# Kernel optimization log

Hardware: AMD Instinct MI355X
Metric: run time of the kernel (lower is better)

The kernel has to match this reference:

```python
import jax, jax.numpy as jnp
import numpy as np

B, S, D, H = 4, 2048, 1024, 16
HD = D // H


def setup_inputs() -> dict:
    key = jax.random.key(0)
    k1, k2, k3 = jax.random.split(key, 3)
    x = jax.random.normal(k1, (B, S, D), dtype=jnp.float32)
    w_qkv = jax.random.normal(k2, (D, 3 * D), dtype=jnp.float32) * (1.0 / np.sqrt(D))
    w_out = jax.random.normal(k3, (D, D), dtype=jnp.float32) * (1.0 / np.sqrt(D))
    return {"x": x, "w_qkv": w_qkv, "w_out": w_out}


def reference(x, w_qkv, w_out):
    bsz, seq_len, d = x.shape
    qkv = x @ w_qkv  # [B, S, 3D]
    q, k, v = jnp.split(qkv, 3, axis=-1)
    # [B, H, S, HD]
    q = q.reshape(bsz, seq_len, H, HD).transpose(0, 2, 1, 3)
    k = k.reshape(bsz, seq_len, H, HD).transpose(0, 2, 1, 3)
    v = v.reshape(bsz, seq_len, H, HD).transpose(0, 2, 1, 3)
    scale = 1.0 / np.sqrt(HD)
    scores = jnp.einsum('bhqd,bhkd->bhqk', q, k) * scale  # [B, H, S, S]
    causal = jnp.tril(jnp.ones((seq_len, seq_len), dtype=bool))
    scores = jnp.where(causal[None, None], scores, -jnp.inf)
    weights = jax.nn.softmax(scores, axis=-1)
    ctx = jnp.einsum('bhqk,bhkd->bhqd', weights, v)
    ctx = ctx.transpose(0, 2, 1, 3).reshape(bsz, seq_len, d)
    return ctx @ w_out
```

## Files before the change

### kernel.cpp

```cpp
#include <hip/hip_runtime.h>
#include <stdint.h>

typedef unsigned short u16;
typedef __attribute__((ext_vector_type(4))) float f32x4;
typedef __attribute__((ext_vector_type(8))) __bf16 bf16x8;
typedef __attribute__((ext_vector_type(8))) u16 u16x8;
typedef __attribute__((ext_vector_type(4))) u16 u16x4;
typedef __attribute__((ext_vector_type(2))) unsigned u32x2;

static constexpr int kB = 4, kS = 2048, kD = 1024, kH = 16, kHD = 64;
static constexpr int M1 = kB * kS;
static constexpr int N1 = 3 * kD;
static constexpr int K1 = kD;

#define SCLF 0.18033688011112042f
#define MFMA16(a, b, c) __builtin_amdgcn_mfma_f32_16x16x32_bf16((a), (b), (c), 0, 0, 0)

union U4 { unsigned u[4]; bf16x8 v; };

__device__ __forceinline__ u16 f2bf(float f) {
  union { float f; uint32_t u; } c; c.f = f;
  uint32_t u = c.u + 0x7FFFu + ((c.u >> 16) & 1u);
  return (u16)(u >> 16);
}

__device__ __forceinline__ unsigned pkbf(float a, float b) {
  union { __bf16 h[2]; unsigned u; } c;
  c.h[0] = (__bf16)a; c.h[1] = (__bf16)b;
  return c.u;
}

__device__ __forceinline__ void gload_lds16(const u16* g, u16* l) {
  __builtin_amdgcn_global_load_lds(
      (const __attribute__((address_space(1))) unsigned int*)g,
      (__attribute__((address_space(3))) unsigned int*)l, 16, 0, 0);
}

__global__ __launch_bounds__(256) void k_cast_x(const float* __restrict__ x,
                                                u16* __restrict__ o) {
  int i = (blockIdx.x * 256 + threadIdx.x) * 4;
  f32x4 v = *(const f32x4*)(x + i);
  u16x4 r;
  r[0] = f2bf(v[0]); r[1] = f2bf(v[1]); r[2] = f2bf(v[2]); r[3] = f2bf(v[3]);
  *(u16x4*)(o + i) = r;
}

__global__ __launch_bounds__(256) void k_transpose_cast(const float* __restrict__ w,
                                                        u16* __restrict__ wt,
                                                        int K, int N) {
  __shared__ float t[32][33];
  const int n0 = blockIdx.x * 32, k0 = blockIdx.y * 32;
  const int tx = threadIdx.x & 31, ty = threadIdx.x >> 5;
  for (int r = ty; r < 32; r += 8)
    t[r][tx] = w[(size_t)(k0 + r) * N + n0 + tx];
  __syncthreads();
  for (int r = ty; r < 32; r += 8)
    wt[(size_t)(n0 + r) * K + k0 + tx] = f2bf(t[tx][r]);
}

template <int MODE>
__global__ __launch_bounds__(512) void k_gemm_bt(const u16* __restrict__ A,
                                                 const u16* __restrict__ BT,
                                                 u16* __restrict__ obf,
                                                 float* __restrict__ of,
                                                 int M, int N, int K) {
  __shared__ __align__(16) u16 Asb[3][128 * 64];
  __shared__ __align__(16) u16 Bsb[3][256 * 64];

  const int tid = threadIdx.x;
  const int wave = tid >> 6, lane = tid & 63;
  const int l15 = lane & 15, l16 = lane >> 4;

  const int bid = blockIdx.x;
  const int qch = gridDim.x >> 3;
  const int swz = (bid & 7) * qch + (bid >> 3);
  const int ntN = N >> 8;
  const int row0 = (swz / ntN) * 128, col0 = (swz % ntN) * 256;
  const int wm = (wave >> 2) * 64, wn = (wave & 3) * 64;

  f32x4 acc[4][4];
#pragma unroll
  for (int i = 0; i < 4; ++i)
#pragma unroll
    for (int j = 0; j < 4; ++j) acc[i][j] = f32x4{0.f, 0.f, 0.f, 0.f};

  const int lr = lane >> 3, ls = lane & 7;
  const u16* srcA[2];
#pragma unroll
  for (int j = 0; j < 2; ++j) {
    const int r = (wave * 2 + j) * 8 + lr;
    srcA[j] = A + (size_t)(row0 + r) * K + (ls ^ (r & 7)) * 8;
  }
  const u16* srcB[4];
#pragma unroll
  for (int j = 0; j < 4; ++j) {
    const int r = (wave * 4 + j) * 8 + lr;
    srcB[j] = BT + (size_t)(col0 + r) * K + (ls ^ (r & 7)) * 8;
  }

  const int nT = K >> 6;

#define STAGE(t)                                                        \
  {                                                                     \
    const int buf_ = (t) % 3;                                           \
    const int kt_ = (t) * 64;                                           \
    _Pragma("unroll")                                                   \
    for (int j = 0; j < 2; ++j)                                         \
      gload_lds16(srcA[j] + kt_, &Asb[buf_][(wave * 2 + j) * 512]);     \
    _Pragma("unroll")                                                   \
    for (int j = 0; j < 4; ++j)                                         \
      gload_lds16(srcB[j] + kt_, &Bsb[buf_][(wave * 4 + j) * 512]);     \
  }

  STAGE(0);
  STAGE(1);

  for (int t = 0; t < nT; ++t) {
    if (t + 1 < nT) asm volatile("s_waitcnt vmcnt(6)" ::: "memory");
    else            asm volatile("s_waitcnt vmcnt(0)" ::: "memory");
    __builtin_amdgcn_s_barrier();
    __builtin_amdgcn_sched_barrier(0);

    if (t + 2 < nT) STAGE(t + 2);

    const u16* As = &Asb[t % 3][0];
    const u16* Bs = &Bsb[t % 3][0];
#pragma unroll
    for (int kk = 0; kk < 2; ++kk) {
      bf16x8 af[4], bfv[4];
#pragma unroll
      for (int f = 0; f < 4; ++f) {
        const int ra = wm + f * 16 + l15;
        af[f] = *(const bf16x8*)&As[ra * 64 + (((kk * 4 + l16) ^ (ra & 7)) * 8)];
        const int rb = wn + f * 16 + l15;
        bfv[f] = *(const bf16x8*)&Bs[rb * 64 + (((kk * 4 + l16) ^ (rb & 7)) * 8)];
      }
      __builtin_amdgcn_s_setprio(1);
#pragma unroll
      for (int fm = 0; fm < 4; ++fm)
#pragma unroll
        for (int fn = 0; fn < 4; ++fn)
          acc[fm][fn] = MFMA16(af[fm], bfv[fn], acc[fm][fn]);
      __builtin_amdgcn_s_setprio(0);
    }
  }

#pragma unroll
  for (int fm = 0; fm < 4; ++fm)
#pragma unroll
    for (int fn = 0; fn < 4; ++fn) {
      const int n = col0 + wn + fn * 16 + l15;
#pragma unroll
      for (int j = 0; j < 4; ++j) {
        const int m = row0 + wm + fm * 16 + l16 * 4 + j;
        float v = acc[fm][fn][j];
        if constexpr (MODE == 0) {
          const int which = n >> 10, d = n & 1023;
          const int h = d >> 6, hd = d & 63;
          const int b = m >> 11, s = m & 2047;
          if (which == 0) v *= SCLF;
          obf[((((size_t)which * 4 + b) * 16 + h) * 2048 + s) * 64 + hd] = f2bf(v);
        } else {
          of[(size_t)m * N + n] = v;
        }
      }
    }
#undef STAGE
}

__global__ __launch_bounds__(512, 4) void k_attn(const u16* __restrict__ Qg,
                                                 const u16* __restrict__ Kg,
                                                 const u16* __restrict__ Vg,
                                                 u16* __restrict__ ctx) {
  __shared__ __align__(16) u16 Ks[2][64 * 64];
  __shared__ __align__(16) unsigned Vt[2][2048];
  __shared__ __align__(16) unsigned Pl[8 * 256];

  const int bid = blockIdx.x;
  const int xcd = bid & 7, i2 = bid >> 3;
  const int bh = xcd * 8 + (i2 & 7);
  const int p = i2 >> 3;
  const int bb = bh >> 4, hh = bh & 15;
  const int tid = threadIdx.x;
  const int wave = tid >> 6, lane = tid & 63;
  const int l15 = lane & 15, l16 = lane >> 4;

  const u16* Qb = Qg + (size_t)bh * kS * kHD;
  const u16* Kb = Kg + (size_t)bh * kS * kHD;
  const u16* Vb = Vg + (size_t)bh * kS * kHD;

  const int kkey = tid >> 3, ksl = tid & 7;
  const int do4 = tid & 15, kp = tid >> 4;
  unsigned* Pw = Pl + wave * 256 + l15 * 16;
  const int pm = ((l15 >> 1) & 3) << 2;

  unsigned voff[4];
#pragma unroll
  for (int i = 0; i < 4; ++i) {
    const int d = do4 * 4 + i;
    voff[i] = d * 32 + (kp ^ ((((d & 7) ^ (d >> 3))) << 2));
  }
  const u16* ksrc = Kb + (size_t)kkey * 64 + (ksl ^ (kkey & 7)) * 8;

  for (int phase = 0; phase < 2; ++phase) {
    const int qsup = phase ? (15 - p) : p;
    const int qstart = qsup * 128 + wave * 16;
    const int ntiles = 2 * qsup + 2;

    bf16x8 bq[2];
#pragma unroll
    for (int ds = 0; ds < 2; ++ds)
      bq[ds] = *(const bf16x8*)(Qb + (size_t)(qstart + l15) * 64 + ds * 32 + l16 * 8);

    f32x4 acc[4];
#pragma unroll
    for (int i = 0; i < 4; ++i) acc[i] = f32x4{0.f, 0.f, 0.f, 0.f};
    float mrow = -3e38f, lrowh = 0.f;

    __syncthreads();

    u16x4 va, vb;
    {
      const u16* vs = Vb + (size_t)(2 * kp) * 64 + do4 * 4;
      va = *(const u16x4*)vs; vb = *(const u16x4*)(vs + 64);
    }
#pragma unroll
    for (int i = 0; i < 4; ++i)
      Vt[0][voff[i]] = (unsigned)va[i] | ((unsigned)vb[i] << 16);
    {
      const u16* vs = Vb + (size_t)(64 + 2 * kp) * 64 + do4 * 4;
      va = *(const u16x4*)vs; vb = *(const u16x4*)(vs + 64);
    }
    gload_lds16(ksrc, &Ks[0][wave * 512]);

    for (int t = 0; t < ntiles; ++t) {
      const int kv0 = t * 64;
      __syncthreads();

      if (t + 1 < ntiles) {
        const int nb = (t + 1) & 1;
#pragma unroll
        for (int i = 0; i < 4; ++i)
          Vt[nb][voff[i]] = (unsigned)va[i] | ((unsigned)vb[i] << 16);
        gload_lds16(ksrc + (size_t)(t + 1) * 64 * 64, &Ks[nb][wave * 512]);
        if (t + 2 < ntiles) {
          const u16* vs = Vb + (size_t)((t + 2) * 64 + 2 * kp) * 64 + do4 * 4;
          va = *(const u16x4*)vs; vb = *(const u16x4*)(vs + 64);
        }
      }

      if (kv0 > qstart + 15) continue;

      const u16* Ksb = &Ks[t & 1][0];
      const unsigned* Vtb = &Vt[t & 1][0];
      const int qv = qstart + l15;
      const bool have1 = (kv0 + 32 <= qstart + 15);

      f32x4 stA0 = f32x4{0.f, 0.f, 0.f, 0.f}, stA1 = stA0;
      f32x4 stB0 = stA0, stB1 = stA0;
      __builtin_amdgcn_s_setprio(1);
#pragma unroll
      for (int ds = 0; ds < 2; ++ds) {
        const int slot = ((ds * 4 + l16) ^ (l15 & 7)) * 8;
        bf16x8 ak0 = *(const bf16x8*)&Ksb[(l15) * 64 + slot];
        stA0 = MFMA16(ak0, bq[ds], stA0);
        bf16x8 ak1 = *(const bf16x8*)&Ksb[(16 + l15) * 64 + slot];
        stA1 = MFMA16(ak1, bq[ds], stA1);
        if (have1) {
          bf16x8 bk0 = *(const bf16x8*)&Ksb[(32 + l15) * 64 + slot];
          stB0 = MFMA16(bk0, bq[ds], stB0);
          bf16x8 bk1 = *(const bf16x8*)&Ksb[(48 + l15) * 64 + slot];
          stB1 = MFMA16(bk1, bq[ds], stB1);
        }
      }
      __builtin_amdgcn_s_setprio(0);

      if (kv0 + 31 > qstart) {
#pragma unroll
        for (int j = 0; j < 4; ++j) {
          const int key = kv0 + l16 * 4 + j;
          stA0[j] = (key <= qv) ? stA0[j] : -3e38f;
          stA1[j] = (key + 16 <= qv) ? stA1[j] : -3e38f;
        }
      }
      if (have1 && (kv0 + 63 > qstart)) {
#pragma unroll
        for (int j = 0; j < 4; ++j) {
          const int key = kv0 + 32 + l16 * 4 + j;
          stB0[j] = (key <= qv) ? stB0[j] : -3e38f;
          stB1[j] = (key + 16 <= qv) ? stB1[j] : -3e38f;
        }
      }

      float tl = fmaxf(fmaxf(fmaxf(stA0[0], stA0[1]), fmaxf(stA0[2], stA0[3])),
                       fmaxf(fmaxf(stA1[0], stA1[1]), fmaxf(stA1[2], stA1[3])));
      if (have1) {
        tl = fmaxf(tl, fmaxf(fmaxf(stB0[0], stB0[1]), fmaxf(stB0[2], stB0[3])));
        tl = fmaxf(tl, fmaxf(fmaxf(stB1[0], stB1[1]), fmaxf(stB1[2], stB1[3])));
      }

      float mn;
      if (__all(tl <= mrow + 8.0f)) {
        mn = mrow;
      } else {
        float tj = fmaxf(tl, __shfl_xor(tl, 16, 64));
        tj = fmaxf(tj, __shfl_xor(tj, 32, 64));
        mn = fmaxf(mrow, tj);
        const float al = exp2f(mrow - mn);
        mrow = mn;
        lrowh *= al;
#pragma unroll
        for (int i = 0; i < 4; ++i)
#pragma unroll
          for (int j = 0; j < 4; ++j) acc[i][j] *= al;
      }

      {
#pragma unroll
        for (int j = 0; j < 4; ++j) {
          stA0[j] = exp2f(stA0[j] - mn);
          stA1[j] = exp2f(stA1[j] - mn);
        }
        lrowh += ((stA0[0] + stA0[1]) + (stA0[2] + stA0[3])) +
                 ((stA1[0] + stA1[1]) + (stA1[2] + stA1[3]));
        const unsigned p0 = pkbf(stA0[0], stA0[1]);
        const unsigned p1 = pkbf(stA0[2], stA0[3]);
        const unsigned p2 = pkbf(stA1[0], stA1[1]);
        const unsigned p3 = pkbf(stA1[2], stA1[3]);
        *(u32x2*)&Pw[(l16 * 2) ^ pm] = u32x2{p0, p1};
        *(u32x2*)&Pw[(8 + l16 * 2) ^ pm] = u32x2{p2, p3};
        U4 f;
        f = *(const U4*)&Pw[(l16 * 4) ^ pm];
        __builtin_amdgcn_s_setprio(1);
#pragma unroll
        for (int dg = 0; dg < 4; ++dg) {
          const int d = dg * 16 + l15;
          const int addr = d * 32 + ((l16 * 4) ^ ((((d & 7) ^ (d >> 3))) << 2));
          const bf16x8 vf = *(const bf16x8*)&Vtb[addr];
          acc[dg] = MFMA16(vf, f.v, acc[dg]);
        }
        __builtin_amdgcn_s_setprio(0);
      }
      if (have1) {
#pragma unroll
        for (int j = 0; j < 4; ++j) {
          stB0[j] = exp2f(stB0[j] - mn);
          stB1[j] = exp2f(stB1[j] - mn);
        }
        lrowh += ((stB0[0] + stB0[1]) + (stB0[2] + stB0[3])) +
                 ((stB1[0] + stB1[1]) + (stB1[2] + stB1[3]));
        const unsigned p0 = pkbf(stB0[0], stB0[1]);
        const unsigned p1 = pkbf(stB0[2], stB0[3]);
        const unsigned p2 = pkbf(stB1[0], stB1[1]);
        const unsigned p3 = pkbf(stB1[2], stB1[3]);
        *(u32x2*)&Pw[(l16 * 2) ^ pm] = u32x2{p0, p1};
        *(u32x2*)&Pw[(8 + l16 * 2) ^ pm] = u32x2{p2, p3};
        U4 f;
        f = *(const U4*)&Pw[(l16 * 4) ^ pm];
        __builtin_amdgcn_s_setprio(1);
#pragma unroll
        for (int dg = 0; dg < 4; ++dg) {
          const int d = dg * 16 + l15;
          const int addr = d * 32 + ((16 + l16 * 4) ^ ((((d & 7) ^ (d >> 3))) << 2));
          const bf16x8 vf = *(const bf16x8*)&Vtb[addr];
          acc[dg] = MFMA16(vf, f.v, acc[dg]);
        }
        __builtin_amdgcn_s_setprio(0);
      }
    }

    float l2 = lrowh + __shfl_xor(lrowh, 16, 64);
    const float lrow = l2 + __shfl_xor(l2, 32, 64);
    const float rl = 1.0f / lrow;
    u16* orow = ctx + ((size_t)bb * kS + (qstart + l15)) * kD + hh * 64;
#pragma unroll
    for (int dg = 0; dg < 4; ++dg) {
      u16x4 pk;
#pragma unroll
      for (int j = 0; j < 4; ++j) pk[j] = f2bf(acc[dg][j] * rl);
      *(u16x4*)&orow[dg * 16 + l16 * 4] = pk;
    }
  }
}

extern "C" void kernel_launch(void* const* d_in, const int* in_sizes, int n_in,
                              void* d_out, int out_size, void* d_ws, size_t ws_size,
                              hipStream_t stream) {
  const float* x     = (const float*)d_in[0];
  const float* w_qkv = (const float*)d_in[1];
  const float* w_out = (const float*)d_in[2];
  float* out = (float*)d_out;

  u16* ws    = (u16*)d_ws;
  u16* x_bf  = ws;
  u16* wqkvT = x_bf + (size_t)M1 * K1;
  u16* woutT = wqkvT + (size_t)N1 * K1;
  u16* qkv   = woutT + (size_t)kD * kD;
  u16* ctx   = qkv + (size_t)3 * kB * kH * kS * kHD;

  k_cast_x<<<M1 * K1 / 1024, 256, 0, stream>>>(x, x_bf);
  k_transpose_cast<<<dim3(N1 / 32, K1 / 32), 256, 0, stream>>>(w_qkv, wqkvT, K1, N1);
  k_transpose_cast<<<dim3(kD / 32, kD / 32), 256, 0, stream>>>(w_out, woutT, kD, kD);

  k_gemm_bt<0><<<dim3(768), 512, 0, stream>>>(x_bf, wqkvT, qkv, nullptr,
                                              M1, N1, K1);

  const u16* Qg = qkv;
  const u16* Kg = qkv + (size_t)kB * kH * kS * kHD;
  const u16* Vg = qkv + (size_t)2 * kB * kH * kS * kHD;
  k_attn<<<dim3(512), 512, 0, stream>>>(Qg, Kg, Vg, ctx);

  k_gemm_bt<1><<<dim3(256), 512, 0, stream>>>(ctx, woutT, nullptr, out,
                                              M1, kD, K1);
}
```

Measured before the change: 203.6 us.

## Merge prep kernels, compute softmax row sums via MFMA, use max3 reductions

```diff
diff --git a/kernel.cpp b/kernel.cpp
--- a/kernel.cpp
+++ b/kernel.cpp
@@ -30,32 +30,43 @@
   return c.u;
 }
 
+__device__ __forceinline__ float max3f(float a, float b, float c) {
+  return fmaxf(fmaxf(a, b), c);
+}
+
 __device__ __forceinline__ void gload_lds16(const u16* g, u16* l) {
   __builtin_amdgcn_global_load_lds(
       (const __attribute__((address_space(1))) unsigned int*)g,
       (__attribute__((address_space(3))) unsigned int*)l, 16, 0, 0);
 }
 
-__global__ __launch_bounds__(256) void k_cast_x(const float* __restrict__ x,
-                                                u16* __restrict__ o) {
-  int i = (blockIdx.x * 256 + threadIdx.x) * 4;
-  f32x4 v = *(const f32x4*)(x + i);
-  u16x4 r;
-  r[0] = f2bf(v[0]); r[1] = f2bf(v[1]); r[2] = f2bf(v[2]); r[3] = f2bf(v[3]);
-  *(u16x4*)(o + i) = r;
-}
-
-__global__ __launch_bounds__(256) void k_transpose_cast(const float* __restrict__ w,
-                                                        u16* __restrict__ wt,
-                                                        int K, int N) {
+__global__ __launch_bounds__(256) void k_prep(const float* __restrict__ x,
+                                              const float* __restrict__ w_qkv,
+                                              const float* __restrict__ w_out,
+                                              u16* __restrict__ x_bf,
+                                              u16* __restrict__ wqkvT,
+                                              u16* __restrict__ woutT) {
+  const int bid = blockIdx.x;
+  if (bid < 8192) {
+    int i = (bid * 256 + threadIdx.x) * 4;
+    f32x4 v = *(const f32x4*)(x + i);
+    u16x4 r;
+    r[0] = f2bf(v[0]); r[1] = f2bf(v[1]); r[2] = f2bf(v[2]); r[3] = f2bf(v[3]);
+    *(u16x4*)(x_bf + i) = r;
+    return;
+  }
   __shared__ float t[32][33];
-  const int n0 = blockIdx.x * 32, k0 = blockIdx.y * 32;
+  const float* w; u16* wt; int N, idx;
+  if (bid < 8192 + 3072) { idx = bid - 8192;  w = w_qkv; wt = wqkvT; N = N1; }
+  else                   { idx = bid - 11264; w = w_out; wt = woutT; N = kD; }
+  const int ntn = N >> 5;
+  const int n0 = (idx % ntn) * 32, k0 = (idx / ntn) * 32;
   const int tx = threadIdx.x & 31, ty = threadIdx.x >> 5;
   for (int r = ty; r < 32; r += 8)
     t[r][tx] = w[(size_t)(k0 + r) * N + n0 + tx];
   __syncthreads();
   for (int r = ty; r < 32; r += 8)
-    wt[(size_t)(n0 + r) * K + k0 + tx] = f2bf(t[tx][r]);
+    wt[(size_t)(n0 + r) * K1 + k0 + tx] = f2bf(t[tx][r]);
 }
 
 template <int MODE>
@@ -194,6 +205,11 @@
   unsigned* Pw = Pl + wave * 256 + l15 * 16;
   const int pm = ((l15 >> 1) & 3) << 2;
 
+  U4 onesu;
+#pragma unroll
+  for (int i = 0; i < 4; ++i) onesu.u[i] = 0x3F803F80u;
+  const bf16x8 vones = onesu.v;
+
   unsigned voff[4];
 #pragma unroll
   for (int i = 0; i < 4; ++i) {
@@ -215,7 +231,8 @@
     f32x4 acc[4];
 #pragma unroll
     for (int i = 0; i < 4; ++i) acc[i] = f32x4{0.f, 0.f, 0.f, 0.f};
-    float mrow = -3e38f, lrowh = 0.f;
+    f32x4 acc_l = f32x4{0.f, 0.f, 0.f, 0.f};
+    float mrow = -3e38f;
 
     __syncthreads();
 
@@ -292,11 +309,16 @@
         }
       }
 
-      float tl = fmaxf(fmaxf(fmaxf(stA0[0], stA0[1]), fmaxf(stA0[2], stA0[3])),
-                       fmaxf(fmaxf(stA1[0], stA1[1]), fmaxf(stA1[2], stA1[3])));
-      if (have1) {
-        tl = fmaxf(tl, fmaxf(fmaxf(stB0[0], stB0[1]), fmaxf(stB0[2], stB0[3])));
-        tl = fmaxf(tl, fmaxf(fmaxf(stB1[0], stB1[1]), fmaxf(stB1[2], stB1[3])));
+      float tl;
+      {
+        const float mA = fmaxf(max3f(stA0[0], stA0[1], stA0[2]),
+                               max3f(stA0[3], stA1[0], stA1[1]));
+        tl = max3f(stA1[2], stA1[3], mA);
+        if (have1) {
+          const float mB = fmaxf(max3f(stB0[0], stB0[1], stB0[2]),
+                                 max3f(stB0[3], stB1[0], stB1[1]));
+          tl = fmaxf(tl, max3f(stB1[2], stB1[3], mB));
+        }
       }
 
       float mn;
@@ -308,7 +330,7 @@
         mn = fmaxf(mrow, tj);
         const float al = exp2f(mrow - mn);
         mrow = mn;
-        lrowh *= al;
+        acc_l[0] *= al;
 #pragma unroll
         for (int i = 0; i < 4; ++i)
 #pragma unroll
@@ -321,8 +343,6 @@
           stA0[j] = exp2f(stA0[j] - mn);
           stA1[j] = exp2f(stA1[j] - mn);
         }
-        lrowh += ((stA0[0] + stA0[1]) + (stA0[2] + stA0[3])) +
-                 ((stA1[0] + stA1[1]) + (stA1[2] + stA1[3]));
         const unsigned p0 = pkbf(stA0[0], stA0[1]);
         const unsigned p1 = pkbf(stA0[2], stA0[3]);
         const unsigned p2 = pkbf(stA1[0], stA1[1]);
@@ -332,6 +352,7 @@
         U4 f;
         f = *(const U4*)&Pw[(l16 * 4) ^ pm];
         __builtin_amdgcn_s_setprio(1);
+        acc_l = MFMA16(vones, f.v, acc_l);
 #pragma unroll
         for (int dg = 0; dg < 4; ++dg) {
           const int d = dg * 16 + l15;
@@ -347,8 +368,6 @@
           stB0[j] = exp2f(stB0[j] - mn);
           stB1[j] = exp2f(stB1[j] - mn);
         }
-        lrowh += ((stB0[0] + stB0[1]) + (stB0[2] + stB0[3])) +
-                 ((stB1[0] + stB1[1]) + (stB1[2] + stB1[3]));
         const unsigned p0 = pkbf(stB0[0], stB0[1]);
         const unsigned p1 = pkbf(stB0[2], stB0[3]);
         const unsigned p2 = pkbf(stB1[0], stB1[1]);
@@ -358,6 +377,7 @@
         U4 f;
         f = *(const U4*)&Pw[(l16 * 4) ^ pm];
         __builtin_amdgcn_s_setprio(1);
+        acc_l = MFMA16(vones, f.v, acc_l);
 #pragma unroll
         for (int dg = 0; dg < 4; ++dg) {
           const int d = dg * 16 + l15;
@@ -369,9 +389,7 @@
       }
     }
 
-    float l2 = lrowh + __shfl_xor(lrowh, 16, 64);
-    const float lrow = l2 + __shfl_xor(l2, 32, 64);
-    const float rl = 1.0f / lrow;
+    const float rl = 1.0f / acc_l[0];
     u16* orow = ctx + ((size_t)bb * kS + (qstart + l15)) * kD + hh * 64;
 #pragma unroll
     for (int dg = 0; dg < 4; ++dg) {
@@ -398,9 +416,7 @@
   u16* qkv   = woutT + (size_t)kD * kD;
   u16* ctx   = qkv + (size_t)3 * kB * kH * kS * kHD;
 
-  k_cast_x<<<M1 * K1 / 1024, 256, 0, stream>>>(x, x_bf);
-  k_transpose_cast<<<dim3(N1 / 32, K1 / 32), 256, 0, stream>>>(w_qkv, wqkvT, K1, N1);
-  k_transpose_cast<<<dim3(kD / 32, kD / 32), 256, 0, stream>>>(w_out, woutT, kD, kD);
+  k_prep<<<dim3(12288), 256, 0, stream>>>(x, w_qkv, w_out, x_bf, wqkvT, woutT);
 
   k_gemm_bt<0><<<dim3(768), 512, 0, stream>>>(x_bf, wqkvT, qkv, nullptr,
                                               M1, N1, K1);
```

Measured after the change: 197.6 us. 1.03x faster.
